# Kernel optimization log

Measured on AMD Instinct MI355X. Metric: run time of the kernel, lower is better.

## Reference

```python
import jax, jax.numpy as jnp
import numpy as np

D_MODEL, D_FF, N_KV, S = 2048, 8192, 256, 16
B, T = 4, 1024


def quantize_w8(w):
    # W8A16 fake quantization with straight-through estimator
    scale = 127.0 / jnp.maximum(jnp.max(jnp.abs(w)), 1e-8)
    w_q = jnp.clip(jnp.round(w * scale), -128, 127) / scale
    return w + jax.lax.stop_gradient(w_q - w)


def setup_inputs() -> dict:
    key = jax.random.key(0)
    ks = jax.random.split(key, 6)
    x = jax.random.normal(ks[0], (B, T, D_MODEL), dtype=jnp.float32)
    indices = jax.random.randint(ks[1], (B, T, S), 0, N_KV, dtype=jnp.int64)
    W_K = jax.random.normal(ks[2], (D_MODEL, N_KV), dtype=jnp.float32) / np.sqrt(D_MODEL)
    W_V = jax.random.normal(ks[3], (D_MODEL, N_KV), dtype=jnp.float32) / np.sqrt(D_MODEL)
    W_in = jax.random.normal(ks[4], (D_MODEL, D_FF), dtype=jnp.float32) / np.sqrt(D_MODEL)
    W_out = jax.random.normal(ks[5], (D_FF, D_MODEL), dtype=jnp.float32) / np.sqrt(D_FF)
    return {"x": x, "indices": indices, "W_K": W_K, "W_V": W_V, "W_in": W_in, "W_out": W_out}


def reference(x, indices, W_K, W_V, W_in, W_out):
    W_K_sim = quantize_w8(W_K)   # [d, 256]
    W_V_sim = quantize_w8(W_V)
    W_in_sim = quantize_w8(W_in)
    W_out_sim = quantize_w8(W_out)
    # F.embedding(indices, W.T): gather rows of W.T -> [b, t, s, d]
    local_K = W_K_sim.T[indices]
    local_V = W_V_sim.T[indices]
    score = jnp.einsum('btd,btsd->bts', x, local_K)
    probs = jax.nn.softmax(score, axis=-1)
    comb_embs = jnp.einsum('bts,btsd->btd', probs, local_V)
    hidden = comb_embs @ W_in_sim           # [b, t, d_ff]
    return hidden @ W_out_sim               # [b, t, d]
```

## Files before the change

### kernel.cpp

```cpp
#include <hip/hip_runtime.h>
#include <hip/hip_bf16.h>

#define D_MODEL 2048
#define D_FF    8192
#define N_KV    256
#define S_TOP   16
#define M_ROWS  4096

typedef __attribute__((ext_vector_type(8))) short bf16x8;
typedef __attribute__((ext_vector_type(4))) float f32x4;
typedef __hip_bfloat16 bf16;

typedef const __attribute__((address_space(1))) unsigned int* gp_t;
typedef __attribute__((address_space(3))) unsigned int* lp_t;

__device__ __forceinline__ void gload16(const void* g, void* l) {
  __builtin_amdgcn_global_load_lds((gp_t)g, (lp_t)l, 16, 0, 0);
}

__global__ __launch_bounds__(256) void maxabs4_kernel(const float4* __restrict__ w0, int n0,
                                                      const float4* __restrict__ w1, int n1,
                                                      const float4* __restrict__ w2, int n2,
                                                      const float4* __restrict__ w3, int n3,
                                                      unsigned* __restrict__ out) {
  const float4* w = blockIdx.y == 0 ? w0 : blockIdx.y == 1 ? w1 : blockIdx.y == 2 ? w2 : w3;
  int n4 = blockIdx.y == 0 ? n0 : blockIdx.y == 1 ? n1 : blockIdx.y == 2 ? n2 : n3;
  float m = 0.f;
  for (long i = (long)blockIdx.x * 256 + threadIdx.x; i < n4; i += (long)gridDim.x * 256) {
    float4 v = w[i];
    m = fmaxf(m, fmaxf(fmaxf(fabsf(v.x), fabsf(v.y)), fmaxf(fabsf(v.z), fabsf(v.w))));
  }
#pragma unroll
  for (int o = 32; o; o >>= 1) m = fmaxf(m, __shfl_down(m, o, 64));
  __shared__ float sm[4];
  int lane = threadIdx.x & 63, wid = threadIdx.x >> 6;
  if (lane == 0) sm[wid] = m;
  __syncthreads();
  if (threadIdx.x == 0) {
    float mm = fmaxf(fmaxf(sm[0], sm[1]), fmaxf(sm[2], sm[3]));
    atomicMax(out + blockIdx.y, __float_as_uint(mm));
  }
}

__global__ __launch_bounds__(256) void quantT_f32(const float* __restrict__ in,
                                                  float* __restrict__ out, int R, int C,
                                                  const unsigned* __restrict__ maxbits) {
  __shared__ float tile[64][65];
  float scale = 127.f / fmaxf(__uint_as_float(*maxbits), 1e-8f);
  int r0 = blockIdx.y << 6, c0 = blockIdx.x << 6;
  int tx = threadIdx.x & 63, ty = threadIdx.x >> 6;
#pragma unroll
  for (int i = 0; i < 16; ++i) {
    int r = ty + (i << 2);
    float v = in[(long)(r0 + r) * C + c0 + tx];
    tile[r][tx] = fminf(fmaxf(rintf(v * scale), -128.f), 127.f);
  }
  __syncthreads();
#pragma unroll
  for (int i = 0; i < 16; ++i) {
    int c = ty + (i << 2);
    out[(long)(c0 + c) * R + r0 + tx] = tile[tx][c] / scale;
  }
}

__global__ __launch_bounds__(256) void quantT_bf16(const float* __restrict__ in,
                                                   bf16* __restrict__ out, int R, int C,
                                                   const unsigned* __restrict__ maxbits) {
  __shared__ float tile[64][65];
  float scale = 127.f / fmaxf(__uint_as_float(*maxbits), 1e-8f);
  int r0 = blockIdx.y << 6, c0 = blockIdx.x << 6;
  int tx = threadIdx.x & 63, ty = threadIdx.x >> 6;
#pragma unroll
  for (int i = 0; i < 16; ++i) {
    int r = ty + (i << 2);
    float v = in[(long)(r0 + r) * C + c0 + tx];
    tile[r][tx] = fminf(fmaxf(rintf(v * scale), -128.f), 127.f);
  }
  __syncthreads();
#pragma unroll
  for (int i = 0; i < 16; ++i) {
    int c = ty + (i << 2);
    out[(long)(c0 + c) * R + r0 + tx] = __float2bfloat16(tile[tx][c]);
  }
}

__global__ __launch_bounds__(256) void attn_kernel(const float* __restrict__ x,
                                                   const int* __restrict__ idx,
                                                   const float* __restrict__ KqT,
                                                   const float* __restrict__ VqT,
                                                   bf16* __restrict__ combHi) {
  int bt = blockIdx.x;
  const float* xr = x + (long)bt * D_MODEL;
  __shared__ int sidx[S_TOP];
  __shared__ float sred[S_TOP][4];
  __shared__ float sp[S_TOP];
  int t = threadIdx.x, lane = t & 63, wid = t >> 6;
  if (t < S_TOP) sidx[t] = idx[(long)bt * S_TOP + t];
  __syncthreads();
  float xv[8];
#pragma unroll
  for (int j = 0; j < 8; ++j) xv[j] = xr[t + (j << 8)];
#pragma unroll
  for (int s = 0; s < S_TOP; ++s) {
    const float* kc = KqT + (long)sidx[s] * D_MODEL;
    float a = 0.f;
#pragma unroll
    for (int j = 0; j < 8; ++j) a += xv[j] * kc[t + (j << 8)];
#pragma unroll
    for (int o = 32; o; o >>= 1) a += __shfl_down(a, o, 64);
    if (lane == 0) sred[s][wid] = a;
  }
  __syncthreads();
  if (t < S_TOP) {
    float sc = sred[t][0] + sred[t][1] + sred[t][2] + sred[t][3];
    float mx = sc;
#pragma unroll
    for (int o = 8; o; o >>= 1) mx = fmaxf(mx, __shfl_xor(mx, o, 16));
    float e = __expf(sc - mx);
    float su = e;
#pragma unroll
    for (int o = 8; o; o >>= 1) su += __shfl_xor(su, o, 16);
    sp[t] = e / su;
  }
  __syncthreads();
  float p[S_TOP];
#pragma unroll
  for (int s = 0; s < S_TOP; ++s) p[s] = sp[s];
#pragma unroll
  for (int j = 0; j < 8; ++j) {
    int d = t + (j << 8);
    float c = 0.f;
#pragma unroll
    for (int s = 0; s < S_TOP; ++s) c += p[s] * VqT[(long)sidx[s] * D_MODEL + d];
    combHi[(long)bt * D_MODEL + d] = __float2bfloat16(c);
  }
}

template <int KT, bool SPLITK, typename OutT>
__global__ __launch_bounds__(512, 2) void gemm8(const bf16* __restrict__ A,
                                                const bf16* __restrict__ B,
                                                const unsigned* maxbits,
                                                OutT* __restrict__ out, int Ntot) {
  __shared__ char lds[131072];
  const int t = threadIdx.x, lane = t & 63, wid = t >> 6;
  const int wr = wid >> 2, wc = wid & 3;
  const int gx = gridDim.x, nwg = gx * gridDim.y;
  const int bid = blockIdx.y * gx + blockIdx.x;
  const int swz = (bid & 7) * (nwg >> 3) + (bid >> 3);
  const long m0 = (long)(swz / gx) << 8;
  const long n0 = (long)(swz % gx) << 8;
  const int NT = (SPLITK ? KT / 2 : KT) / 64;
  const bf16* gA = A + m0 * KT + (SPLITK ? blockIdx.z * (KT / 2) : 0);
  const bf16* gB = B + n0 * KT + (SPLITK ? blockIdx.z * (KT / 2) : 0);

  const int srow = t >> 3;
  const int gcol = ((t & 7) ^ (srow & 7)) << 3;
  const int xr = (lane & 7) << 4;
  const int arow = lane & 15;
  const int kcolb = (lane >> 4) << 4;

  f32x4 acc[8][4] = {};

#define STAGE(mat, h, j, c)                                                          \
  {                                                                                  \
    const bf16* _g = (mat ? gB : gA) + (long)((h)*128) * KT + (long)(j)*64 + gcol;   \
    char* _l = lds + (mat)*65536 + (c)*32768 + (h)*16384;                            \
    gload16(_g + (long)srow * KT, _l + (t << 4));                                    \
    gload16(_g + (long)(64 + srow) * KT, _l + 8192 + (t << 4));                      \
  }

  STAGE(0, 0, 0, 0) STAGE(0, 1, 0, 0) STAGE(1, 0, 0, 0) STAGE(1, 1, 0, 0)

  bf16x8 aF[4][2], bF[4][2];

  for (int j = 0; j < NT; ++j) {
    const int c = j & 1;
    const char* lA = lds + c * 32768;
    const char* lB = lds + 65536 + c * 32768;
    asm volatile("s_waitcnt vmcnt(2)" ::: "memory");
    __builtin_amdgcn_s_barrier();
#pragma unroll
    for (int m = 0; m < 4; ++m)
#pragma unroll
      for (int ks = 0; ks < 2; ++ks)
        aF[m][ks] = *(const bf16x8*)(lA + (wr * 128 + m * 16 + arow) * 128 +
                                     ((ks * 64 + kcolb) ^ xr));
#pragma unroll
    for (int n = 0; n < 2; ++n)
#pragma unroll
      for (int ks = 0; ks < 2; ++ks)
        bF[n][ks] = *(const bf16x8*)(lB + (wc * 64 + n * 16 + arow) * 128 +
                                     ((ks * 64 + kcolb) ^ xr));
    if (j + 1 < NT) { STAGE(0, 0, j + 1, c ^ 1) STAGE(0, 1, j + 1, c ^ 1) }
    __builtin_amdgcn_s_setprio(1);
#pragma unroll
    for (int m = 0; m < 4; ++m)
#pragma unroll
      for (int n = 0; n < 2; ++n)
#pragma unroll
        for (int ks = 0; ks < 2; ++ks)
          acc[m][n] = __builtin_amdgcn_mfma_f32_16x16x32_bf16(aF[m][ks], bF[n][ks], acc[m][n], 0, 0, 0);
    __builtin_amdgcn_s_setprio(0);
    if (j + 1 < NT) { asm volatile("s_waitcnt vmcnt(4)" ::: "memory"); }
    else           { asm volatile("s_waitcnt vmcnt(0)" ::: "memory"); }
    __builtin_amdgcn_s_barrier();
#pragma unroll
    for (int n = 0; n < 2; ++n)
#pragma unroll
      for (int ks = 0; ks < 2; ++ks)
        bF[2 + n][ks] = *(const bf16x8*)(lB + (wc * 64 + (2 + n) * 16 + arow) * 128 +
                                         ((ks * 64 + kcolb) ^ xr));
    if (j + 1 < NT) { STAGE(1, 0, j + 1, c ^ 1) STAGE(1, 1, j + 1, c ^ 1) }
    __builtin_amdgcn_s_setprio(1);
#pragma unroll
    for (int m = 0; m < 4; ++m)
#pragma unroll
      for (int n = 0; n < 2; ++n)
#pragma unroll
        for (int ks = 0; ks < 2; ++ks)
          acc[m][2 + n] = __builtin_amdgcn_mfma_f32_16x16x32_bf16(aF[m][ks], bF[2 + n][ks], acc[m][2 + n], 0, 0, 0);
    __builtin_amdgcn_s_setprio(0);
#pragma unroll
    for (int m = 0; m < 4; ++m)
#pragma unroll
      for (int ks = 0; ks < 2; ++ks)
        aF[m][ks] = *(const bf16x8*)(lA + (wr * 128 + (4 + m) * 16 + arow) * 128 +
                                     ((ks * 64 + kcolb) ^ xr));
    __builtin_amdgcn_s_setprio(1);
#pragma unroll
    for (int m = 0; m < 4; ++m)
#pragma unroll
      for (int n = 0; n < 2; ++n)
#pragma unroll
        for (int ks = 0; ks < 2; ++ks)
          acc[4 + m][n] = __builtin_amdgcn_mfma_f32_16x16x32_bf16(aF[m][ks], bF[n][ks], acc[4 + m][n], 0, 0, 0);
    __builtin_amdgcn_s_setprio(0);
    __builtin_amdgcn_s_setprio(1);
#pragma unroll
    for (int m = 0; m < 4; ++m)
#pragma unroll
      for (int n = 0; n < 2; ++n)
#pragma unroll
        for (int ks = 0; ks < 2; ++ks)
          acc[4 + m][2 + n] = __builtin_amdgcn_mfma_f32_16x16x32_bf16(aF[m][ks], bF[2 + n][ks], acc[4 + m][2 + n], 0, 0, 0);
    __builtin_amdgcn_s_setprio(0);
  }
#undef STAGE

  float inv = fmaxf(__uint_as_float(*(volatile const unsigned*)maxbits), 1e-8f) * (1.f / 127.f);
#pragma unroll
  for (int m = 0; m < 8; ++m)
#pragma unroll
    for (int n = 0; n < 4; ++n)
#pragma unroll
      for (int r = 0; r < 4; ++r) {
        long row = m0 + wr * 128 + m * 16 + ((lane >> 4) << 2) + r;
        long col = n0 + wc * 64 + n * 16 + (lane & 15);
        float h = acc[m][n][r] * inv;
        if constexpr (SPLITK)
          atomicAdd(&out[row * Ntot + col], h);
        else if constexpr (__is_same(OutT, float))
          out[row * Ntot + col] = h;
        else
          out[row * Ntot + col] = __float2bfloat16(h);
      }
}

extern "C" void kernel_launch(void* const* d_in, const int* in_sizes, int n_in, void* d_out,
                              int out_size, void* d_ws, size_t ws_size, hipStream_t stream) {
  const float* x = (const float*)d_in[0];
  const int* idx = (const int*)d_in[1];
  const float* W_K = (const float*)d_in[2];
  const float* W_V = (const float*)d_in[3];
  const float* W_in = (const float*)d_in[4];
  const float* W_out = (const float*)d_in[5];
  float* out = (float*)d_out;

  char* ws = (char*)d_ws;
  size_t off = 0;
  unsigned* maxb = (unsigned*)(ws + off); off += 256;
  float* KqT = (float*)(ws + off); off += (size_t)N_KV * D_MODEL * 4;
  float* VqT = (float*)(ws + off); off += (size_t)N_KV * D_MODEL * 4;
  bf16* QinT = (bf16*)(ws + off); off += (size_t)D_FF * D_MODEL * 2;
  bf16* combHi = (bf16*)(ws + off);
  bf16* QoutT = (bf16*)(ws + off);
  off += (size_t)D_MODEL * D_FF * 2;
  bf16* hidHi = (bf16*)(ws + off); off += (size_t)M_ROWS * D_FF * 2;

  hipMemsetAsync(maxb, 0, 16, stream);
  hipMemsetAsync(out, 0, (size_t)M_ROWS * D_MODEL * 4, stream);
  maxabs4_kernel<<<dim3(512, 4), 256, 0, stream>>>(
      (const float4*)W_K, (D_MODEL * N_KV) / 4, (const float4*)W_V, (D_MODEL * N_KV) / 4,
      (const float4*)W_in, (D_MODEL * D_FF) / 4, (const float4*)W_out, (D_FF * D_MODEL) / 4,
      maxb);

  quantT_f32<<<dim3(N_KV / 64, D_MODEL / 64), 256, 0, stream>>>(W_K, KqT, D_MODEL, N_KV, maxb + 0);
  quantT_f32<<<dim3(N_KV / 64, D_MODEL / 64), 256, 0, stream>>>(W_V, VqT, D_MODEL, N_KV, maxb + 1);
  quantT_bf16<<<dim3(D_FF / 64, D_MODEL / 64), 256, 0, stream>>>(W_in, QinT, D_MODEL, D_FF, maxb + 2);

  attn_kernel<<<M_ROWS, 256, 0, stream>>>(x, idx, KqT, VqT, combHi);

  gemm8<D_MODEL, false, bf16><<<dim3(D_FF / 256, M_ROWS / 256), 512, 0, stream>>>(
      combHi, QinT, maxb + 2, hidHi, D_FF);

  quantT_bf16<<<dim3(D_MODEL / 64, D_FF / 64), 256, 0, stream>>>(W_out, QoutT, D_FF, D_MODEL, maxb + 3);

  gemm8<D_FF, true, float><<<dim3(D_MODEL / 256, M_ROWS / 256, 2), 512, 0, stream>>>(
      hidHi, QoutT, maxb + 3, out, D_MODEL);
}
```

Before: 452.9 us.

## Restructure GEMM main loop into 8-phase ping-pong schedule with interleaved warp tiles

```diff
diff --git a/kernel.cpp b/kernel.cpp
--- a/kernel.cpp
+++ b/kernel.cpp
@@ -17,6 +17,8 @@
 __device__ __forceinline__ void gload16(const void* g, void* l) {
   __builtin_amdgcn_global_load_lds((gp_t)g, (lp_t)l, 16, 0, 0);
 }
+
+#define CFENCE asm volatile("" ::: "memory")
 
 __global__ __launch_bounds__(256) void maxabs4_kernel(const float4* __restrict__ w0, int n0,
                                                       const float4* __restrict__ w1, int n1,
@@ -168,84 +170,132 @@
     gload16(_g + (long)srow * KT, _l + (t << 4));                                    \
     gload16(_g + (long)(64 + srow) * KT, _l + 8192 + (t << 4));                      \
   }
-
-  STAGE(0, 0, 0, 0) STAGE(0, 1, 0, 0) STAGE(1, 0, 0, 0) STAGE(1, 1, 0, 0)
-
-  bf16x8 aF[4][2], bF[4][2];
-
-  for (int j = 0; j < NT; ++j) {
-    const int c = j & 1;
-    const char* lA = lds + c * 32768;
-    const char* lB = lds + 65536 + c * 32768;
-    asm volatile("s_waitcnt vmcnt(2)" ::: "memory");
+#define LDA(buf, h, mf, ks)                                                          \
+  (*(const bf16x8*)(lds + (buf)*32768 + (h)*16384 +                                  \
+                    ((mf)*32 + wr * 16 + arow) * 128 + (((ks)*64 + kcolb) ^ xr)))
+#define LDB(buf, h, nf, ks)                                                          \
+  (*(const bf16x8*)(lds + 65536 + (buf)*32768 + (h)*16384 +                          \
+                    ((nf)*64 + wc * 16 + arow) * 128 + (((ks)*64 + kcolb) ^ xr)))
+#define MFMA_Q(AF, BF, ro, co)                                                       \
+  _Pragma("unroll") for (int m = 0; m < 4; ++m)                                      \
+  _Pragma("unroll") for (int n = 0; n < 2; ++n)                                      \
+  _Pragma("unroll") for (int ks = 0; ks < 2; ++ks)                                   \
+    acc[(ro) + m][(co) + n] =                                                        \
+        __builtin_amdgcn_mfma_f32_16x16x32_bf16(AF[m][ks], BF[n][ks], acc[(ro) + m][(co) + n], 0, 0, 0);
+#define PH_SYNC                                                                      \
+  CFENCE; __builtin_amdgcn_s_barrier();                                              \
+  asm volatile("s_waitcnt lgkmcnt(0)" ::: "memory");                                 \
+  __builtin_amdgcn_sched_barrier(0);
+#define PH_END CFENCE; __builtin_amdgcn_s_barrier(); CFENCE;
+
+  STAGE(0, 0, 0, 0) STAGE(1, 0, 0, 0) STAGE(0, 1, 0, 0) STAGE(1, 1, 0, 0)
+  STAGE(0, 0, 1, 1) STAGE(1, 0, 1, 1) STAGE(0, 1, 1, 1)
+  asm volatile("s_waitcnt vmcnt(6)" ::: "memory");
+  __builtin_amdgcn_s_barrier();
+
+  bf16x8 aF[4][2], b0F[2][2], b1F[2][2];
+
+  for (int T = 0; T < NT; T += 2) {
+    const bool last = (T + 2 >= NT);
+#pragma unroll
+    for (int m = 0; m < 4; ++m)
+#pragma unroll
+      for (int ks = 0; ks < 2; ++ks) aF[m][ks] = LDA(0, 0, m, ks);
+#pragma unroll
+    for (int n = 0; n < 2; ++n)
+#pragma unroll
+      for (int ks = 0; ks < 2; ++ks) b0F[n][ks] = LDB(0, 0, n, ks);
+    STAGE(1, 1, T + 1, 1)
+    asm volatile("s_waitcnt lgkmcnt(8)" ::: "memory");
+    PH_SYNC
+    __builtin_amdgcn_s_setprio(1);
+    MFMA_Q(aF, b0F, 0, 0)
+    __builtin_amdgcn_s_setprio(0);
+    PH_END
+#pragma unroll
+    for (int n = 0; n < 2; ++n)
+#pragma unroll
+      for (int ks = 0; ks < 2; ++ks) b1F[n][ks] = LDB(0, 1, n, ks);
+    if (!last) STAGE(0, 0, T + 2, 0)
+    PH_SYNC
+    __builtin_amdgcn_s_setprio(1);
+    MFMA_Q(aF, b1F, 0, 2)
+    __builtin_amdgcn_s_setprio(0);
+    PH_END
+#pragma unroll
+    for (int m = 0; m < 4; ++m)
+#pragma unroll
+      for (int ks = 0; ks < 2; ++ks) aF[m][ks] = LDA(0, 1, m, ks);
+    if (!last) STAGE(1, 0, T + 2, 0)
+    PH_SYNC
+    __builtin_amdgcn_s_setprio(1);
+    MFMA_Q(aF, b0F, 4, 0)
+    __builtin_amdgcn_s_setprio(0);
+    PH_END
+    if (!last) {
+      STAGE(0, 1, T + 2, 0)
+      asm volatile("s_waitcnt vmcnt(6)" ::: "memory");
+    } else {
+      asm volatile("s_waitcnt vmcnt(0)" ::: "memory");
+    }
     __builtin_amdgcn_s_barrier();
+    __builtin_amdgcn_s_setprio(1);
+    MFMA_Q(aF, b1F, 4, 2)
+    __builtin_amdgcn_s_setprio(0);
+    PH_END
 #pragma unroll
     for (int m = 0; m < 4; ++m)
 #pragma unroll
-      for (int ks = 0; ks < 2; ++ks)
-        aF[m][ks] = *(const bf16x8*)(lA + (wr * 128 + m * 16 + arow) * 128 +
-                                     ((ks * 64 + kcolb) ^ xr));
+      for (int ks = 0; ks < 2; ++ks) aF[m][ks] = LDA(1, 0, m, ks);
 #pragma unroll
     for (int n = 0; n < 2; ++n)
 #pragma unroll
-      for (int ks = 0; ks < 2; ++ks)
-        bF[n][ks] = *(const bf16x8*)(lB + (wc * 64 + n * 16 + arow) * 128 +
-                                     ((ks * 64 + kcolb) ^ xr));
-    if (j + 1 < NT) { STAGE(0, 0, j + 1, c ^ 1) STAGE(0, 1, j + 1, c ^ 1) }
-    __builtin_amdgcn_s_setprio(1);
+      for (int ks = 0; ks < 2; ++ks) b0F[n][ks] = LDB(1, 0, n, ks);
+    if (!last) STAGE(1, 1, T + 2, 0)
+    asm volatile("s_waitcnt lgkmcnt(8)" ::: "memory");
+    PH_SYNC
+    __builtin_amdgcn_s_setprio(1);
+    MFMA_Q(aF, b0F, 0, 0)
+    __builtin_amdgcn_s_setprio(0);
+    PH_END
+#pragma unroll
+    for (int n = 0; n < 2; ++n)
+#pragma unroll
+      for (int ks = 0; ks < 2; ++ks) b1F[n][ks] = LDB(1, 1, n, ks);
+    if (!last) STAGE(0, 0, T + 3, 1)
+    PH_SYNC
+    __builtin_amdgcn_s_setprio(1);
+    MFMA_Q(aF, b1F, 0, 2)
+    __builtin_amdgcn_s_setprio(0);
+    PH_END
 #pragma unroll
     for (int m = 0; m < 4; ++m)
 #pragma unroll
-      for (int n = 0; n < 2; ++n)
-#pragma unroll
-        for (int ks = 0; ks < 2; ++ks)
-          acc[m][n] = __builtin_amdgcn_mfma_f32_16x16x32_bf16(aF[m][ks], bF[n][ks], acc[m][n], 0, 0, 0);
-    __builtin_amdgcn_s_setprio(0);
-    if (j + 1 < NT) { asm volatile("s_waitcnt vmcnt(4)" ::: "memory"); }
-    else           { asm volatile("s_waitcnt vmcnt(0)" ::: "memory"); }
+      for (int ks = 0; ks < 2; ++ks) aF[m][ks] = LDA(1, 1, m, ks);
+    if (!last) STAGE(1, 0, T + 3, 1)
+    PH_SYNC
+    __builtin_amdgcn_s_setprio(1);
+    MFMA_Q(aF, b0F, 4, 0)
+    __builtin_amdgcn_s_setprio(0);
+    PH_END
+    if (!last) {
+      STAGE(0, 1, T + 3, 1)
+      asm volatile("s_waitcnt vmcnt(6)" ::: "memory");
+    } else {
+      asm volatile("s_waitcnt vmcnt(0)" ::: "memory");
+    }
     __builtin_amdgcn_s_barrier();
-#pragma unroll
-    for (int n = 0; n < 2; ++n)
-#pragma unroll
-      for (int ks = 0; ks < 2; ++ks)
-        bF[2 + n][ks] = *(const bf16x8*)(lB + (wc * 64 + (2 + n) * 16 + arow) * 128 +
-                                         ((ks * 64 + kcolb) ^ xr));
-    if (j + 1 < NT) { STAGE(1, 0, j + 1, c ^ 1) STAGE(1, 1, j + 1, c ^ 1) }
-    __builtin_amdgcn_s_setprio(1);
-#pragma unroll
-    for (int m = 0; m < 4; ++m)
-#pragma unroll
-      for (int n = 0; n < 2; ++n)
-#pragma unroll
-        for (int ks = 0; ks < 2; ++ks)
-          acc[m][2 + n] = __builtin_amdgcn_mfma_f32_16x16x32_bf16(aF[m][ks], bF[2 + n][ks], acc[m][2 + n], 0, 0, 0);
-    __builtin_amdgcn_s_setprio(0);
-#pragma unroll
-    for (int m = 0; m < 4; ++m)
-#pragma unroll
-      for (int ks = 0; ks < 2; ++ks)
-        aF[m][ks] = *(const bf16x8*)(lA + (wr * 128 + (4 + m) * 16 + arow) * 128 +
-                                     ((ks * 64 + kcolb) ^ xr));
-    __builtin_amdgcn_s_setprio(1);
-#pragma unroll
-    for (int m = 0; m < 4; ++m)
-#pragma unroll
-      for (int n = 0; n < 2; ++n)
-#pragma unroll
-        for (int ks = 0; ks < 2; ++ks)
-          acc[4 + m][n] = __builtin_amdgcn_mfma_f32_16x16x32_bf16(aF[m][ks], bF[n][ks], acc[4 + m][n], 0, 0, 0);
-    __builtin_amdgcn_s_setprio(0);
-    __builtin_amdgcn_s_setprio(1);
-#pragma unroll
-    for (int m = 0; m < 4; ++m)
-#pragma unroll
-      for (int n = 0; n < 2; ++n)
-#pragma unroll
-        for (int ks = 0; ks < 2; ++ks)
-          acc[4 + m][2 + n] = __builtin_amdgcn_mfma_f32_16x16x32_bf16(aF[m][ks], bF[2 + n][ks], acc[4 + m][2 + n], 0, 0, 0);
-    __builtin_amdgcn_s_setprio(0);
+    __builtin_amdgcn_s_setprio(1);
+    MFMA_Q(aF, b1F, 4, 2)
+    __builtin_amdgcn_s_setprio(0);
+    PH_END
   }
 #undef STAGE
+#undef LDA
+#undef LDB
+#undef MFMA_Q
+#undef PH_SYNC
+#undef PH_END
 
   float inv = fmaxf(__uint_as_float(*(volatile const unsigned*)maxbits), 1e-8f) * (1.f / 127.f);
 #pragma unroll
@@ -254,8 +304,8 @@
     for (int n = 0; n < 4; ++n)
 #pragma unroll
       for (int r = 0; r < 4; ++r) {
-        long row = m0 + wr * 128 + m * 16 + ((lane >> 4) << 2) + r;
-        long col = n0 + wc * 64 + n * 16 + (lane & 15);
+        long row = m0 + (m & 3) * 32 + (m >> 2) * 128 + wr * 16 + ((lane >> 4) << 2) + r;
+        long col = n0 + (n & 1) * 64 + (n >> 1) * 128 + wc * 16 + (lane & 15);
         float h = acc[m][n][r] * inv;
         if constexpr (SPLITK)
           atomicAdd(&out[row * Ntot + col], h);
```

After: 464.3 us. 1.03x slower.
